# Optimization experiments

Measured on AMD Instinct MI355X. Metric: run time of the kernel, lower is better.

## Reference

```python
import jax, jax.numpy as jnp
import numpy as np

L, B, E, H = 1024, 8, 1024, 16


def setup_inputs() -> dict:
    key = jax.random.key(0)
    k1, k2, k3, k4, k5 = jax.random.split(key, 5)
    scale = 1.0 / np.sqrt(E)
    return {
        "x": jax.random.normal(k1, (L, B, E), dtype=jnp.float32),
        "in_proj_weight": jax.random.normal(k2, (3 * E, E), dtype=jnp.float32) * scale,
        "in_proj_bias": jax.random.normal(k3, (3 * E,), dtype=jnp.float32) * 0.01,
        "out_proj_weight": jax.random.normal(k4, (E, E), dtype=jnp.float32) * scale,
        "out_proj_bias": jax.random.normal(k5, (E,), dtype=jnp.float32) * 0.01,
        "num_heads": H,
    }


def reference(x, in_proj_weight, in_proj_bias, out_proj_weight, out_proj_bias, num_heads):
    # x: [L, B, E] (tgt_len, batch, embed_dim), self-attention path of
    # multi_head_attention_func (no masks, no bias_k/v, no add_zero_attn,
    # dropout_p=0 / eval mode).
    Lq, Bq, Eq = x.shape
    hd = Eq // num_heads
    scaling = float(hd) ** -0.5
    # fused qkv projection: linear(x, in_proj_weight, in_proj_bias).chunk(3)
    qkv = x @ in_proj_weight.T + in_proj_bias  # [L, B, 3E]
    q, k, v = jnp.split(qkv, 3, axis=-1)
    q = q * scaling
    def to_heads(t):  # [L, B, E] -> [B*H, L, hd]
        return t.reshape(Lq, Bq * num_heads, hd).transpose(1, 0, 2)
    q, k, v = to_heads(q), to_heads(k), to_heads(v)
    # explicit QK^T -> softmax -> PV (naive attention, as in the source)
    scores = jnp.einsum('bqd,bkd->bqk', q, k)      # [B*H, L, L]
    attn = jax.nn.softmax(scores, axis=-1)
    out = jnp.einsum('bqk,bkd->bqd', attn, v)      # [B*H, L, hd]
    out = out.transpose(1, 0, 2).reshape(Lq, Bq, Eq)
    out = out @ out_proj_weight.T + out_proj_bias  # [L, B, E]
    return out
```

## Files before the change

kernel.cpp:

```cpp
#include <hip/hip_runtime.h>

#define L_DIM 1024
#define B_DIM 8
#define E_DIM 1024
#define H_DIM 16
#define HD 64
#define BH_DIM (B_DIM * H_DIM)

typedef float f32x4 __attribute__((ext_vector_type(4)));
typedef _Float16 f16_t;
typedef f16_t f16x4 __attribute__((ext_vector_type(4)));
typedef f16_t f16x8 __attribute__((ext_vector_type(8)));

static __device__ __forceinline__ void gld16(const void* g, void* l) {
  __builtin_amdgcn_global_load_lds(
      (const __attribute__((address_space(1))) unsigned int*)g,
      (__attribute__((address_space(3))) unsigned int*)l, 16, 0, 0);
}

__global__ __launch_bounds__(256) void convert_f16(
    const float* __restrict__ x, const float* __restrict__ wi,
    const float* __restrict__ wo, f16_t* __restrict__ x16,
    f16_t* __restrict__ wi16, f16_t* __restrict__ wo16) {
  const int NX = (L_DIM * B_DIM * E_DIM) / 4;
  const int NWI = (3 * E_DIM * E_DIM) / 4;
  const int NWO = (E_DIM * E_DIM) / 4;
  const int total = NX + NWI + NWO;
  for (int i = blockIdx.x * blockDim.x + threadIdx.x; i < total;
       i += gridDim.x * blockDim.x) {
    const float4* src; f16_t* dst; int j;
    if (i < NX)            { src = (const float4*)x;  dst = x16;  j = i; }
    else if (i < NX + NWI) { src = (const float4*)wi; dst = wi16; j = i - NX; }
    else                   { src = (const float4*)wo; dst = wo16; j = i - NX - NWI; }
    const float4 v = src[j];
    f16x4 h = {(f16_t)v.x, (f16_t)v.y, (f16_t)v.z, (f16_t)v.w};
    *(f16x4*)(dst + (size_t)j * 4) = h;
  }
}


#define GQ_FENCE asm volatile("" ::: "memory")
#define GQ_BARRIER do { GQ_FENCE; __builtin_amdgcn_s_barrier(); GQ_FENCE; } while (0)
#define GQ_LGKM0 do { asm volatile("s_waitcnt lgkmcnt(0)" ::: "memory"); \
                      __builtin_amdgcn_sched_barrier(0); } while (0)
#define GQ_VMCNT4 asm volatile("s_waitcnt vmcnt(4)" ::: "memory")

#define STAGE_A(d, ht, kt) do {                                              \
    gld16(Asrc + (size_t)(ht) * (128 * 1024) + (kt) * 64,                    \
          &As[(d) * 16384 + (ht) * 8192 + tid * 8]);                         \
    gld16(Asrc + (size_t)(ht) * (128 * 1024) + 64 * 1024 + (kt) * 64,        \
          &As[(d) * 16384 + (ht) * 8192 + 4096 + tid * 8]);                  \
  } while (0)
#define STAGE_B(d, ht, kt) do {                                              \
    gld16(Bsrc + (size_t)(ht) * (128 * 1024) + (kt) * 64,                    \
          &Bs[(d) * 16384 + (ht) * 8192 + tid * 8]);                         \
    gld16(Bsrc + (size_t)(ht) * (128 * 1024) + 64 * 1024 + (kt) * 64,        \
          &Bs[(d) * 16384 + (ht) * 8192 + 4096 + tid * 8]);                  \
  } while (0)

static __device__ __forceinline__ const f16x8* fp16frag(
    const f16_t* tile, int r, int ks, int quad, int l16) {
  const int bo = (r * 128 + ks * 64 + quad * 16) ^ ((l16 & 7) << 4);
  return (const f16x8*)((const char*)tile + bo);
}

#define GQ_PHASE(d, g, STAGE_STMT, ENDWAIT) do {                             \
    f16x8 af_[2][2];                                                         \
    _Pragma("unroll") for (int f_ = 0; f_ < 2; ++f_)                         \
      _Pragma("unroll") for (int ks_ = 0; ks_ < 2; ++ks_)                    \
        af_[f_][ks_] = *fp16frag(&As[(d) * 16384],                           \
            wr * 128 + ((g) * 2 + f_) * 16 + l16, ks_, quad, l16);           \
    if ((g) == 0) {                                                          \
      _Pragma("unroll") for (int c_ = 0; c_ < 4; ++c_)                       \
        _Pragma("unroll") for (int ks_ = 0; ks_ < 2; ++ks_)                  \
          bf[c_][ks_] = *fp16frag(&Bs[(d) * 16384],                          \
              wc * 64 + c_ * 16 + l16, ks_, quad, l16);                      \
    }                                                                        \
    STAGE_STMT;                                                              \
    GQ_BARRIER;                                                              \
    GQ_LGKM0;                                                                \
    __builtin_amdgcn_s_setprio(1);                                           \
    _Pragma("unroll") for (int f_ = 0; f_ < 2; ++f_)                         \
      _Pragma("unroll") for (int c_ = 0; c_ < 4; ++c_)                       \
        _Pragma("unroll") for (int ks_ = 0; ks_ < 2; ++ks_)                  \
          acc[(g) * 2 + f_][c_] = __builtin_amdgcn_mfma_f32_16x16x32_f16(    \
              af_[f_][ks_], bf[c_][ks_], acc[(g) * 2 + f_][c_], 0, 0, 0);    \
    __builtin_amdgcn_s_setprio(0);                                           \
    ENDWAIT;                                                                 \
    GQ_BARRIER;                                                              \
  } while (0)

__global__ __launch_bounds__(512, 2) void gemm_qkv(
    const f16_t* __restrict__ A, const f16_t* __restrict__ B,
    const float* __restrict__ bias, f16_t* __restrict__ Oq,
    f16_t* __restrict__ Ok, f16_t* __restrict__ Ov) {
  constexpr int K = 1024;
  constexpr int NT = K / 64;
  __shared__ __align__(16) f16_t As[2 * 16384];
  __shared__ __align__(16) f16_t Bs[2 * 16384];

  const int tid = threadIdx.x;
  const int lane = tid & 63;
  const int w = tid >> 6;
  const int wr = w >> 2;
  const int wc = w & 3;
  const int quad = lane >> 4;
  const int l16 = lane & 15;

  const int bid = blockIdx.x;
  const int wg = (bid & 7) * 48 + (bid >> 3);
  const int tn = wg >> 5;
  const int tm = wg & 31;
  const int m0 = tm * 256;
  const int n0 = tn * 256;

  const int srow = tid >> 3;
  const int scol = ((tid & 7) ^ (srow & 7)) * 8;
  const f16_t* Asrc = A + (size_t)(m0 + srow) * K + scol;
  const f16_t* Bsrc = B + (size_t)(n0 + srow) * K + scol;

  f32x4 acc[8][4] = {};
  f16x8 bf[4][2];

  STAGE_A(0, 0, 0); STAGE_A(0, 1, 0);
  STAGE_B(0, 0, 0); STAGE_B(0, 1, 0);
  STAGE_B(1, 0, 1); STAGE_B(1, 1, 1);
  GQ_VMCNT4;
  GQ_BARRIER;

  for (int it = 0; it < 8; ++it) {
    const int t1 = 2 * it + 1;
    const int ta = (2 * it + 2 < NT) ? 2 * it + 2 : NT - 1;
    const int tb = (2 * it + 3 < NT) ? 2 * it + 3 : NT - 1;
    GQ_PHASE(0, 0, STAGE_A(1, 0, t1), );
    GQ_PHASE(0, 1, STAGE_A(1, 1, t1), );
    GQ_PHASE(0, 2, STAGE_B(0, 0, ta), );
    GQ_PHASE(0, 3, STAGE_B(0, 1, ta), GQ_VMCNT4);
    GQ_PHASE(1, 0, STAGE_A(0, 0, ta), );
    GQ_PHASE(1, 1, STAGE_A(0, 1, ta), );
    GQ_PHASE(1, 2, STAGE_B(1, 0, tb), );
    GQ_PHASE(1, 3, STAGE_B(1, 1, tb), GQ_VMCNT4);
  }

#pragma unroll
  for (int i = 0; i < 8; ++i) {
    const int mbase = m0 + wr * 128 + i * 16 + quad * 4;
#pragma unroll
    for (int c = 0; c < 4; ++c) {
      const int n = n0 + wc * 64 + c * 16 + l16;
      const float bv = bias[n];
      const int chunk = n >> 10;
      const int e = n & 1023;
      const int h = e >> 6;
      const int d = e & 63;
#pragma unroll
      for (int r = 0; r < 4; ++r) {
        const int m = mbase + r;
        const int l = m >> 3, b = m & 7;
        const size_t idx = ((size_t)(b * H_DIM + h) * L_DIM + l) * HD + d;
        const float val = acc[i][c][r] + bv;
        if (chunk == 0)      Oq[idx] = (f16_t)(val * 0.125f);
        else if (chunk == 1) Ok[idx] = (f16_t)val;
        else                 Ov[idx] = (f16_t)val;
      }
    }
  }
}

template <int MODE>
__global__ __launch_bounds__(256, 2) void gemm_f16(
    const f16_t* __restrict__ A, const f16_t* __restrict__ B,
    const float* __restrict__ bias, void* __restrict__ O0v,
    void* __restrict__ O1v, void* __restrict__ O2v) {
  constexpr int K = 1024;
  __shared__ __align__(16) f16_t As[128 * 32];
  __shared__ __align__(16) f16_t Bs[128 * 32];

  const int tid = threadIdx.x;
  const int lane = tid & 63;
  const int wave = tid >> 6;
  const int wm = (wave & 1) * 64;
  const int wn = (wave >> 1) * 64;
  const int quad = lane >> 4;
  const int l16 = lane & 15;
  const int m0 = blockIdx.y * 128;
  const int n0 = blockIdx.x * 128;

  const int cr = tid >> 2;
  const int cc = (tid & 3) * 8;

  f32x4 acc[4][4] = {};

  for (int k0 = 0; k0 < K; k0 += 32) {
    __syncthreads();
    gld16(A + (size_t)(m0 + cr) * K + k0 + cc,      As + tid * 8);
    gld16(A + (size_t)(m0 + 64 + cr) * K + k0 + cc, As + 2048 + tid * 8);
    gld16(B + (size_t)(n0 + cr) * K + k0 + cc,      Bs + tid * 8);
    gld16(B + (size_t)(n0 + 64 + cr) * K + k0 + cc, Bs + 2048 + tid * 8);
    __syncthreads();

    f16x8 af[4], bfr[4];
#pragma unroll
    for (int t = 0; t < 4; ++t) {
      af[t]  = *(const f16x8*)&As[(wm + t * 16 + l16) * 32 + quad * 8];
      bfr[t] = *(const f16x8*)&Bs[(wn + t * 16 + l16) * 32 + quad * 8];
    }
#pragma unroll
    for (int i = 0; i < 4; ++i)
#pragma unroll
      for (int j = 0; j < 4; ++j)
        acc[i][j] = __builtin_amdgcn_mfma_f32_16x16x32_f16(af[i], bfr[j], acc[i][j], 0, 0, 0);
  }

#pragma unroll
  for (int i = 0; i < 4; ++i) {
    const int mbase = m0 + wm + i * 16 + quad * 4;
#pragma unroll
    for (int j = 0; j < 4; ++j) {
      const int n = n0 + wn + j * 16 + l16;
      const float bv = bias[n];
      if (MODE == 0) {
        f16_t* O0 = (f16_t*)O0v; f16_t* O1 = (f16_t*)O1v; f16_t* O2 = (f16_t*)O2v;
        const int chunk = n >> 10;
        const int e = n & 1023;
        const int h = e >> 6;
        const int d = e & 63;
#pragma unroll
        for (int r = 0; r < 4; ++r) {
          const int m = mbase + r;
          const int l = m >> 3, b = m & 7;
          const size_t idx = ((size_t)(b * H_DIM + h) * L_DIM + l) * HD + d;
          const float val = acc[i][j][r] + bv;
          if (chunk == 0)      O0[idx] = (f16_t)(val * 0.125f);
          else if (chunk == 1) O1[idx] = (f16_t)val;
          else                 O2[idx] = (f16_t)val;
        }
      } else {
        float* O0 = (float*)O0v;
#pragma unroll
        for (int r = 0; r < 4; ++r) {
          const int m = mbase + r;
          O0[(size_t)m * E_DIM + n] = acc[i][j][r] + bv;
        }
      }
    }
  }
}

__global__ __launch_bounds__(256, 2) void attn_f16(
    const f16_t* __restrict__ Q, const f16_t* __restrict__ K,
    const f16_t* __restrict__ V, f16_t* __restrict__ O) {
  constexpr int KSTR = 70;
  __shared__ __align__(16) f16_t Ks[64 * KSTR];
  __shared__ __align__(16) f16_t Vs[64 * KSTR];
  __shared__ float Ls[4][64];

  const int tid = threadIdx.x;
  const int lane = tid & 63;
  const int w = tid >> 6;
  const int quad = lane >> 4;
  const int l16 = lane & 15;
  const int bh = blockIdx.y;
  const int q0 = blockIdx.x * 256 + w * 64;

  const f16_t* Qb = Q + (size_t)bh * L_DIM * HD;
  const f16_t* Kb = K + (size_t)bh * L_DIM * HD;
  const f16_t* Vb = V + (size_t)bh * L_DIM * HD;

  f16x8 qf[4][2];
#pragma unroll
  for (int nt = 0; nt < 4; ++nt)
#pragma unroll
    for (int kc = 0; kc < 2; ++kc)
      qf[nt][kc] = *(const f16x8*)(Qb + (size_t)(q0 + nt * 16 + l16) * HD + kc * 32 + quad * 8);

  f32x4 oacc[4][4] = {};
  float rsum[4] = {0.0f, 0.0f, 0.0f, 0.0f};

  const int sr = tid >> 3;
  const int sc8 = (tid & 7) * 8;
  const int va = tid & 31;
  const int vg = tid >> 5;
  const int rA = (l16 >> 2) * 8 + (l16 & 3);

  for (int kt = 0; kt < 16; ++kt) {
    __syncthreads();
    {
      const f16_t* kp = Kb + (size_t)(kt * 64) * HD;
#pragma unroll
      for (int rr = 0; rr < 2; ++rr) {
        const int row = sr + rr * 32;
        *(f16x8*)&Ks[row * KSTR + sc8] = *(const f16x8*)(kp + (size_t)row * HD + sc8);
      }
      const f16_t* vp = Vb + (size_t)(kt * 64 + vg * 8) * HD + 2 * va;
      unsigned int vd[8];
#pragma unroll
      for (int i = 0; i < 8; ++i) vd[i] = *(const unsigned int*)(vp + (size_t)i * HD);
      union { unsigned int u[4]; f16x8 v; } lo, hi;
#pragma unroll
      for (int i = 0; i < 4; ++i) {
        lo.u[i] = (vd[2 * i] & 0xffffu) | (vd[2 * i + 1] << 16);
        hi.u[i] = (vd[2 * i] >> 16) | (vd[2 * i + 1] & 0xffff0000u);
      }
      *(f16x8*)&Vs[(2 * va) * KSTR + vg * 8] = lo.v;
      *(f16x8*)&Vs[(2 * va + 1) * KSTR + vg * 8] = hi.v;
    }
    __syncthreads();

#pragma unroll
    for (int c = 0; c < 2; ++c) {
      f32x4 sc[2][4] = {};
#pragma unroll
      for (int h = 0; h < 2; ++h) {
        const int row = c * 32 + h * 4 + rA;
#pragma unroll
        for (int kc = 0; kc < 2; ++kc) {
          const f16x8 ka = *(const f16x8*)&Ks[row * KSTR + kc * 32 + quad * 8];
#pragma unroll
          for (int nt = 0; nt < 4; ++nt)
            sc[h][nt] = __builtin_amdgcn_mfma_f32_16x16x32_f16(ka, qf[nt][kc], sc[h][nt], 0, 0, 0);
        }
      }

      f16x8 pa[4];
#pragma unroll
      for (int nt = 0; nt < 4; ++nt)
#pragma unroll
        for (int h = 0; h < 2; ++h)
#pragma unroll
          for (int r = 0; r < 4; ++r) {
            const float e = __expf(sc[h][nt][r]);
            rsum[nt] += e;
            pa[nt][h * 4 + r] = (f16_t)e;
          }

#pragma unroll
      for (int nd = 0; nd < 4; ++nd) {
        const f16x8 vb = *(const f16x8*)&Vs[(nd * 16 + l16) * KSTR + c * 32 + quad * 8];
#pragma unroll
        for (int nt = 0; nt < 4; ++nt)
          oacc[nt][nd] = __builtin_amdgcn_mfma_f32_16x16x32_f16(pa[nt], vb, oacc[nt][nd], 0, 0, 0);
      }
    }
  }

#pragma unroll
  for (int nt = 0; nt < 4; ++nt) {
    float rs = rsum[nt];
    rs += __shfl_xor(rs, 16); rs += __shfl_xor(rs, 32);
    if (quad == 0) Ls[w][nt * 16 + l16] = rs;
  }
  asm volatile("s_waitcnt lgkmcnt(0)" ::: "memory");

  const int b = bh >> 4;
  const int h = bh & 15;
#pragma unroll
  for (int nt = 0; nt < 4; ++nt)
#pragma unroll
    for (int r = 0; r < 4; ++r) {
      const int ql = nt * 16 + quad * 4 + r;
      const float inv = 1.0f / Ls[w][ql];
      const int qrow = q0 + ql;
#pragma unroll
      for (int nd = 0; nd < 4; ++nd) {
        const int d = nd * 16 + l16;
        O[((size_t)qrow * B_DIM + b) * E_DIM + h * HD + d] = (f16_t)(oacc[nt][nd][r] * inv);
      }
    }
}

extern "C" void kernel_launch(void* const* d_in, const int* in_sizes, int n_in,
                              void* d_out, int out_size, void* d_ws, size_t ws_size,
                              hipStream_t stream) {
  const float* x     = (const float*)d_in[0];
  const float* w_in  = (const float*)d_in[1];
  const float* b_in  = (const float*)d_in[2];
  const float* w_out = (const float*)d_in[3];
  const float* b_out = (const float*)d_in[4];

  const size_t TS = (size_t)BH_DIM * L_DIM * HD;
  f16_t* q16  = (f16_t*)d_ws;
  f16_t* k16  = q16 + TS;
  f16_t* v16  = k16 + TS;
  f16_t* x16  = v16 + TS;
  f16_t* wi16 = x16 + TS;
  f16_t* wo16 = wi16 + (size_t)3 * E_DIM * E_DIM;
  f16_t* ao16 = x16;

  convert_f16<<<4096, 256, 0, stream>>>(x, w_in, w_out, x16, wi16, wo16);
  gemm_qkv<<<384, 512, 0, stream>>>(x16, wi16, b_in, q16, k16, v16);
  attn_f16<<<dim3(4, 128), 256, 0, stream>>>(q16, k16, v16, ao16);
  gemm_f16<1><<<dim3(8, 64), 256, 0, stream>>>(ao16, wo16, b_out, d_out, nullptr, nullptr);
}
```

Baseline: 240.7 us.

## Software-pipeline LDS fragment reads with double-buffered registers in QKV GEMM

Restructures the QKV GEMM main loop so that A and B fragments for the next phase are read from LDS into alternate register sets while the current phase's MFMAs run. Full lgkmcnt(0) waits become partial waits, and one of the two barriers per phase is removed. This targets LDS read latency exposed before each MFMA block, at the cost of extra VGPRs for the doubled fragment buffers and fragile hand-tuned vmcnt/lgkmcnt counts that could cause races if miscounted.

Result: slower. 290.7 us (+20.8%).

```diff
diff --git a/kernel.cpp b/kernel.cpp
--- a/kernel.cpp
+++ b/kernel.cpp
@@ -39,11 +39,9 @@
 }
 
 
-#define GQ_FENCE asm volatile("" ::: "memory")
-#define GQ_BARRIER do { GQ_FENCE; __builtin_amdgcn_s_barrier(); GQ_FENCE; } while (0)
-#define GQ_LGKM0 do { asm volatile("s_waitcnt lgkmcnt(0)" ::: "memory"); \
-                      __builtin_amdgcn_sched_barrier(0); } while (0)
-#define GQ_VMCNT4 asm volatile("s_waitcnt vmcnt(4)" ::: "memory")
+#define LGKM(n) do { asm volatile("s_waitcnt lgkmcnt(" #n ")" ::: "memory");  \
+                     __builtin_amdgcn_sched_barrier(0); } while (0)
+#define VMW(n) asm volatile("s_waitcnt vmcnt(" #n ")" ::: "memory")
 
 #define STAGE_A(d, ht, kt) do {                                              \
     gld16(Asrc + (size_t)(ht) * (128 * 1024) + (kt) * 64,                    \
@@ -64,30 +62,33 @@
   return (const f16x8*)((const char*)tile + bo);
 }
 
-#define GQ_PHASE(d, g, STAGE_STMT, ENDWAIT) do {                             \
-    f16x8 af_[2][2];                                                         \
+#define BFF(nb, bfF, c0) do {                                                \
+    _Pragma("unroll") for (int cc_ = 0; cc_ < 2; ++cc_)                      \
+      _Pragma("unroll") for (int ks_ = 0; ks_ < 2; ++ks_)                    \
+        bfF[(c0) + cc_][ks_] = *fp16frag(&Bs[(nb) * 16384],                  \
+            wc * 64 + ((c0) + cc_) * 16 + l16, ks_, quad, l16);              \
+  } while (0)
+
+#define PH(g, afU, afF, asrc, bfU, BFFILL_STMT, STAGE_STMT, LGW, ENDW) do {  \
     _Pragma("unroll") for (int f_ = 0; f_ < 2; ++f_)                         \
       _Pragma("unroll") for (int ks_ = 0; ks_ < 2; ++ks_)                    \
-        af_[f_][ks_] = *fp16frag(&As[(d) * 16384],                           \
-            wr * 128 + ((g) * 2 + f_) * 16 + l16, ks_, quad, l16);           \
-    if ((g) == 0) {                                                          \
-      _Pragma("unroll") for (int c_ = 0; c_ < 4; ++c_)                       \
-        _Pragma("unroll") for (int ks_ = 0; ks_ < 2; ++ks_)                  \
-          bf[c_][ks_] = *fp16frag(&Bs[(d) * 16384],                          \
-              wc * 64 + c_ * 16 + l16, ks_, quad, l16);                      \
-    }                                                                        \
+        afF[f_][ks_] = *fp16frag(&As[(asrc) * 16384],                        \
+            wr * 128 + (((((g) + 1) & 3) * 2) + f_) * 16 + l16,              \
+            ks_, quad, l16);                                                 \
+    BFFILL_STMT;                                                             \
     STAGE_STMT;                                                              \
-    GQ_BARRIER;                                                              \
-    GQ_LGKM0;                                                                \
+    LGW;                                                                     \
     __builtin_amdgcn_s_setprio(1);                                           \
     _Pragma("unroll") for (int f_ = 0; f_ < 2; ++f_)                         \
       _Pragma("unroll") for (int c_ = 0; c_ < 4; ++c_)                       \
         _Pragma("unroll") for (int ks_ = 0; ks_ < 2; ++ks_)                  \
           acc[(g) * 2 + f_][c_] = __builtin_amdgcn_mfma_f32_16x16x32_f16(    \
-              af_[f_][ks_], bf[c_][ks_], acc[(g) * 2 + f_][c_], 0, 0, 0);    \
+              afU[f_][ks_], bfU[c_][ks_], acc[(g) * 2 + f_][c_], 0, 0, 0);   \
     __builtin_amdgcn_s_setprio(0);                                           \
-    ENDWAIT;                                                                 \
-    GQ_BARRIER;                                                              \
+    __builtin_amdgcn_sched_barrier(0);                                       \
+    ENDW;                                                                    \
+    __builtin_amdgcn_s_barrier();                                            \
+    __builtin_amdgcn_sched_barrier(0);                                       \
   } while (0)
 
 __global__ __launch_bounds__(512, 2) void gemm_qkv(
@@ -120,26 +121,34 @@
   const f16_t* Bsrc = B + (size_t)(n0 + srow) * K + scol;
 
   f32x4 acc[8][4] = {};
-  f16x8 bf[4][2];
+  f16x8 afA[2][2], afB[2][2];
+  f16x8 bfX[4][2], bfY[4][2];
 
   STAGE_A(0, 0, 0); STAGE_A(0, 1, 0);
   STAGE_B(0, 0, 0); STAGE_B(0, 1, 0);
   STAGE_B(1, 0, 1); STAGE_B(1, 1, 1);
-  GQ_VMCNT4;
-  GQ_BARRIER;
+  VMW(4);
+  __builtin_amdgcn_s_barrier();
+  __builtin_amdgcn_sched_barrier(0);
+#pragma unroll
+  for (int f_ = 0; f_ < 2; ++f_)
+#pragma unroll
+    for (int ks_ = 0; ks_ < 2; ++ks_)
+      afA[f_][ks_] = *fp16frag(&As[0], wr * 128 + f_ * 16 + l16, ks_, quad, l16);
+  BFF(0, bfX, 0); BFF(0, bfX, 2);
 
   for (int it = 0; it < 8; ++it) {
     const int t1 = 2 * it + 1;
     const int ta = (2 * it + 2 < NT) ? 2 * it + 2 : NT - 1;
     const int tb = (2 * it + 3 < NT) ? 2 * it + 3 : NT - 1;
-    GQ_PHASE(0, 0, STAGE_A(1, 0, t1), );
-    GQ_PHASE(0, 1, STAGE_A(1, 1, t1), );
-    GQ_PHASE(0, 2, STAGE_B(0, 0, ta), );
-    GQ_PHASE(0, 3, STAGE_B(0, 1, ta), GQ_VMCNT4);
-    GQ_PHASE(1, 0, STAGE_A(0, 0, ta), );
-    GQ_PHASE(1, 1, STAGE_A(0, 1, ta), );
-    GQ_PHASE(1, 2, STAGE_B(1, 0, tb), );
-    GQ_PHASE(1, 3, STAGE_B(1, 1, tb), GQ_VMCNT4);
+    PH(0, afA, afB, 0, bfX, , STAGE_A(1, 0, t1), LGKM(4), );
+    PH(1, afB, afA, 0, bfX, , STAGE_A(1, 1, t1), LGKM(4), VMW(4));
+    PH(2, afA, afB, 0, bfX, BFF(1, bfY, 0), STAGE_B(0, 0, ta), LGKM(8), VMW(2));
+    PH(3, afB, afA, 1, bfX, BFF(1, bfY, 2), STAGE_B(0, 1, ta), LGKM(8), );
+    PH(0, afA, afB, 1, bfY, , STAGE_A(0, 0, ta), LGKM(4), );
+    PH(1, afB, afA, 1, bfY, , STAGE_A(0, 1, ta), LGKM(4), VMW(4));
+    PH(2, afA, afB, 1, bfY, BFF(0, bfX, 0), STAGE_B(1, 0, tb), LGKM(8), VMW(2));
+    PH(3, afB, afA, 0, bfY, BFF(0, bfX, 2), STAGE_B(1, 1, tb), LGKM(8), );
   }
 
 #pragma unroll
```
